# Performance work log

Measured on AMD Instinct MI355X. Metric: run time of the kernel, lower is better.

## Reference

```python
import jax, jax.numpy as jnp
import numpy as np

K = 3  # reassembly kernel size (hardcoded in module)
S = 2  # upsample scale (hardcoded)
PAD = K // 2


def _nearest_up2(t):
    # F.interpolate(scale_factor=2, mode='nearest') on NCHW
    return jnp.repeat(jnp.repeat(t, 2, axis=2), 2, axis=3)


def _patches3x3(t):
    # F.unfold(kernel=3, pad=1) -> [B, C, 9, H, W], k = ki*3 + kj (row-major)
    B, C, H, W = t.shape
    tp = jnp.pad(t, ((0, 0), (0, 0), (PAD, PAD), (PAD, PAD)))
    return jnp.stack([tp[:, :, i:i + H, j:j + W] for i in range(K) for j in range(K)], axis=2)


def setup_inputs() -> dict:
    key = jax.random.key(0)
    k1, k2 = jax.random.split(key)
    x = jax.random.normal(k1, (2, 256, 128, 128), dtype=jnp.float32)
    W_off = jax.random.normal(k2, (2, 1, 5, 5), dtype=jnp.float32) * 1e-3  # normal_init std=0.001
    b_off = jnp.zeros((2,), dtype=jnp.float32)
    return {"x": x, "W_off": W_off, "b_off": b_off}


def reference(x, W_off, b_off):
    B, C, H, W = x.shape
    H2, W2 = S * H, S * W

    mean = jnp.mean(x, axis=1, keepdims=True)  # [B,1,H,W]

    # offset = tanh(conv5x5(nearest_up2(mean))) / 4 -> [B,2,2H,2W]
    mean_up = _nearest_up2(mean)
    off = jax.lax.conv_general_dilated(mean_up, W_off, (1, 1), ((2, 2), (2, 2)))
    offset = jnp.tanh(off + b_off[None, :, None, None]) / 4.0

    # center buffer: pixel_shuffle of [1,8,1,1]; per 2x2 cell, channel 0 varies with j, channel 1 with i
    cell = jnp.array([[[-0.25, 0.25], [-0.25, 0.25]],
                      [[-0.25, -0.25], [0.25, 0.25]]], dtype=x.dtype)  # [2(ch),2(i),2(j)]
    center = jnp.broadcast_to(cell[:, None, :, None, :], (2, H, 2, W, 2)).reshape(2, H2, W2)

    shift = center[None] + offset  # [B,2,2H,2W]

    # neighbor grid: n0 (fast, width) = [-1,0,1]*3 ; n1 (slow, height) = repeat([-1,0,1],3)
    n0 = jnp.tile(jnp.array([-1.0, 0.0, 1.0], dtype=x.dtype), 3)        # [9]
    n1 = jnp.repeat(jnp.array([-1.0, 0.0, 1.0], dtype=x.dtype), 3)      # [9]
    d2 = (shift[:, 0:1] - n0[None, :, None, None]) ** 2 + \
         (shift[:, 1:2] - n1[None, :, None, None]) ** 2                 # [B,9,2H,2W]
    kernels = 1.0 / (d2 + 0.2)

    # grad gating from 3x3 neighborhood of mean
    pm = _patches3x3(mean)[:, 0]            # [B,9,H,W]
    grad = pm - mean                        # broadcast over k
    grad = 1.0 / (grad ** 2 + 1.0)
    logits = _nearest_up2(grad) * kernels   # [B,9,2H,2W]
    kernels = jax.nn.softmax(logits, axis=1)

    # CARAFE: out[b,c,2h+p,2w+q] = sum_k kernels[b,k,2h+p,2w+q] * patches[b,c,k,h,w]
    patches = _patches3x3(x)                        # [B,C,9,H,W]
    Kr = kernels.reshape(B, K * K, H, S, W, S)      # [B,9,H,2,W,2]
    out = jnp.einsum('bkhpwq,bckhw->bchpwq', Kr, patches).reshape(B, C, H2, W2)
    return out
```

## Files before the change

kernel.cpp:

```cpp
#include <hip/hip_runtime.h>
#include <math.h>

#define B 2
#define C 256
#define H 128
#define W 128
#define H2 256
#define W2 256
#define CPT 16
#define TW 16

__global__ __launch_bounds__(1024) void mean_kernel(const float* __restrict__ x,
                                                    float* __restrict__ mean) {
    int bh = blockIdx.x;
    int b = bh / H, h = bh % H;
    int tid = threadIdx.x;
    int g  = tid >> 5;
    int w4 = tid & 31;

    const float4* xb = (const float4*)x + (size_t)b * C * (H * W / 4)
                       + (size_t)h * (W / 4) + w4;
    const size_t cstride = H * W / 4;

    float4 acc = make_float4(0.f, 0.f, 0.f, 0.f);
    #pragma unroll
    for (int i = 0; i < C / 32; ++i) {
        float4 v = xb[(size_t)(g * (C / 32) + i) * cstride];
        acc.x += v.x; acc.y += v.y; acc.z += v.z; acc.w += v.w;
    }

    __shared__ float4 sm[1024];
    sm[tid] = acc;
    __syncthreads();
    for (int s = 16; s >= 1; s >>= 1) {
        if (g < s) {
            float4 o = sm[tid + s * 32];
            acc.x += o.x; acc.y += o.y; acc.z += o.z; acc.w += o.w;
            sm[tid] = acc;
        }
        __syncthreads();
    }
    if (g == 0) {
        const float inv = 1.0f / C;
        float4 m = make_float4(acc.x * inv, acc.y * inv, acc.z * inv, acc.w * inv);
        ((float4*)mean)[(size_t)bh * (W / 4) + w4] = m;
    }
}

__global__ __launch_bounds__(256) void weights_kernel(const float* __restrict__ mean,
                                                      const float* __restrict__ Woff,
                                                      const float* __restrict__ boff,
                                                      float* __restrict__ Kw) {
    __shared__ float sm[10][12];
    __shared__ float sW[50];
    __shared__ float sb[2];

    int b  = blockIdx.z;
    int x0 = blockIdx.x * TW;
    int y0 = blockIdx.y * TW;
    int h0 = y0 >> 1, w0 = x0 >> 1;
    int tid = threadIdx.x;

    if (tid < 100) {
        int lh = tid / 10, lw = tid % 10;
        int hh = h0 - 1 + lh, ww = w0 - 1 + lw;
        sm[lh][lw] = (hh >= 0 && hh < H && ww >= 0 && ww < W)
                         ? mean[(size_t)b * H * W + hh * W + ww] : 0.f;
    }
    if (tid >= 128 && tid < 178) sW[tid - 128] = Woff[tid - 128];
    if (tid >= 192 && tid < 194) sb[tid - 192] = boff[tid - 192];
    __syncthreads();

    int tx = tid & 15, ty = tid >> 4;
    int y = y0 + ty, x = x0 + tx;

    float off0 = 0.f, off1 = 0.f;
    #pragma unroll
    for (int u = 0; u < 5; ++u) {
        int lh = ((y + u - 2) >> 1) - (h0 - 1);
        #pragma unroll
        for (int v = 0; v < 5; ++v) {
            int lw = ((x + v - 2) >> 1) - (w0 - 1);
            float m = sm[lh][lw];
            off0 += m * sW[u * 5 + v];
            off1 += m * sW[25 + u * 5 + v];
        }
    }
    float s0 = tanhf(off0 + sb[0]) * 0.25f + ((x & 1) ? 0.25f : -0.25f);
    float s1 = tanhf(off1 + sb[1]) * 0.25f + ((y & 1) ? 0.25f : -0.25f);

    int lhc = (ty >> 1) + 1;
    int lwc = (tx >> 1) + 1;
    float mc = sm[lhc][lwc];

    float lg[9];
    float mx = -1e30f;
    #pragma unroll
    for (int k = 0; k < 9; ++k) {
        int di = k / 3 - 1, dj = k % 3 - 1;
        float pm = sm[lhc + di][lwc + dj];
        float g = pm - mc;
        float grad = 1.0f / (g * g + 1.0f);
        float d0 = s0 - (float)dj;
        float d1 = s1 - (float)di;
        float kern = 1.0f / (d0 * d0 + d1 * d1 + 0.2f);
        float l = grad * kern;
        lg[k] = l;
        mx = fmaxf(mx, l);
    }
    float sum = 0.f;
    #pragma unroll
    for (int k = 0; k < 9; ++k) { lg[k] = expf(lg[k] - mx); sum += lg[k]; }
    float inv = 1.0f / sum;

    float* o = Kw + (size_t)b * 9 * (H2 * W2) + (size_t)y * W2 + x;
    #pragma unroll
    for (int k = 0; k < 9; ++k) o[(size_t)k * (H2 * W2)] = lg[k] * inv;
}

__global__ __launch_bounds__(256) void carafe_kernel(const float* __restrict__ x,
                                                     const float* __restrict__ Kw,
                                                     float* __restrict__ out) {
    int idx = blockIdx.x * blockDim.x + threadIdx.x;
    int w2 = idx & 63;
    int h  = (idx >> 6) & (H - 1);
    int cg = (idx >> 13) & (C / CPT - 1);
    int b  = idx >> 17;

    int w  = w2 * 2;
    int y0 = 2 * h, x0 = 2 * w;

    const float* kb = Kw + (size_t)b * 9 * (H2 * W2) + (size_t)y0 * W2 + x0;
    float4 wk[2][9];
    #pragma unroll
    for (int k = 0; k < 9; ++k) {
        wk[0][k] = *(const float4*)(kb + (size_t)k * (H2 * W2));
        wk[1][k] = *(const float4*)(kb + (size_t)k * (H2 * W2) + W2);
    }

    int off[3][4]; bool val[3][4];
    #pragma unroll
    for (int r = 0; r < 3; ++r) {
        int hh = h - 1 + r;
        #pragma unroll
        for (int c = 0; c < 4; ++c) {
            int ww = w - 1 + c;
            val[r][c] = (hh >= 0) & (hh < H) & (ww >= 0) & (ww < W);
            off[r][c] = hh * W + ww;
        }
    }

    const float* xb = x   + (size_t)(b * C + cg * CPT) * (H * W);
    float*       ob = out + (size_t)(b * C + cg * CPT) * (H2 * W2)
                          + (size_t)y0 * W2 + x0;

    #pragma unroll 2
    for (int cc = 0; cc < CPT; ++cc) {
        float p[3][4];
        #pragma unroll
        for (int r = 0; r < 3; ++r)
            #pragma unroll
            for (int c = 0; c < 4; ++c)
                p[r][c] = val[r][c] ? xb[off[r][c]] : 0.f;

        #pragma unroll
        for (int pp = 0; pp < 2; ++pp) {
            float4 acc = make_float4(0.f, 0.f, 0.f, 0.f);
            #pragma unroll
            for (int k = 0; k < 9; ++k) {
                int ki = k / 3, kj = k % 3;
                float a  = p[ki][kj];
                float bb = p[ki][kj + 1];
                acc.x += wk[pp][k].x * a;
                acc.y += wk[pp][k].y * a;
                acc.z += wk[pp][k].z * bb;
                acc.w += wk[pp][k].w * bb;
            }
            *(float4*)(ob + (size_t)pp * W2) = acc;
        }
        xb += H * W;
        ob += H2 * W2;
    }
}

extern "C" void kernel_launch(void* const* d_in, const int* in_sizes, int n_in,
                              void* d_out, int out_size, void* d_ws, size_t ws_size,
                              hipStream_t stream) {
    const float* x    = (const float*)d_in[0];
    const float* Woff = (const float*)d_in[1];
    const float* boff = (const float*)d_in[2];
    float* out = (float*)d_out;

    float* mean = (float*)d_ws;
    float* Kw   = mean + (size_t)B * H * W;

    mean_kernel<<<B * H, 1024, 0, stream>>>(x, mean);

    dim3 wgrid(W2 / TW, H2 / TW, B);
    weights_kernel<<<wgrid, 256, 0, stream>>>(mean, Woff, boff, Kw);

    int mt = B * (C / CPT) * H * (W / 2);
    carafe_kernel<<<mt / 256, 256, 0, stream>>>(x, Kw, out);
}
```

Baseline: 176.1 us.

## Use float2 loads with wavefront shuffles for halo, fold boundary masks, nontemporal stores

The CARAFE kernel now loads each input row as one float2 per thread and gets the left and right halo columns from neighbouring lanes via shuffles. Boundary validity is folded into the reassembly weights once, and rows are clamped, so the per-element predicated loads go away. Outputs are written with nontemporal stores so the large output stream does not pollute the cache. The weights kernel switches to hardware reciprocal, fast exp and an exp-based tanh, which trades some accuracy for fewer instructions.

```diff
diff --git a/kernel.cpp b/kernel.cpp
--- a/kernel.cpp
+++ b/kernel.cpp
@@ -10,6 +10,19 @@
 #define CPT 16
 #define TW 16
 
+typedef float vfloat4 __attribute__((ext_vector_type(4)));
+
+__device__ __forceinline__ float frcp(float x) { return __builtin_amdgcn_rcpf(x); }
+__device__ __forceinline__ float fast_tanh(float x) {
+    float e = __expf(2.0f * x);
+    return 1.0f - 2.0f * frcp(e + 1.0f);
+}
+
+__device__ __forceinline__ void nt_store4(float* p, const float4& v) {
+    vfloat4 t; t.x = v.x; t.y = v.y; t.z = v.z; t.w = v.w;
+    __builtin_nontemporal_store(t, (vfloat4*)p);
+}
+
 __global__ __launch_bounds__(1024) void mean_kernel(const float* __restrict__ x,
                                                     float* __restrict__ mean) {
     int bh = blockIdx.x;
@@ -86,8 +99,8 @@
             off1 += m * sW[25 + u * 5 + v];
         }
     }
-    float s0 = tanhf(off0 + sb[0]) * 0.25f + ((x & 1) ? 0.25f : -0.25f);
-    float s1 = tanhf(off1 + sb[1]) * 0.25f + ((y & 1) ? 0.25f : -0.25f);
+    float s0 = fast_tanh(off0 + sb[0]) * 0.25f + ((x & 1) ? 0.25f : -0.25f);
+    float s1 = fast_tanh(off1 + sb[1]) * 0.25f + ((y & 1) ? 0.25f : -0.25f);
 
     int lhc = (ty >> 1) + 1;
     int lwc = (tx >> 1) + 1;
@@ -100,18 +113,18 @@
         int di = k / 3 - 1, dj = k % 3 - 1;
         float pm = sm[lhc + di][lwc + dj];
         float g = pm - mc;
-        float grad = 1.0f / (g * g + 1.0f);
+        float grad = frcp(g * g + 1.0f);
         float d0 = s0 - (float)dj;
         float d1 = s1 - (float)di;
-        float kern = 1.0f / (d0 * d0 + d1 * d1 + 0.2f);
+        float kern = frcp(d0 * d0 + d1 * d1 + 0.2f);
         float l = grad * kern;
         lg[k] = l;
         mx = fmaxf(mx, l);
     }
     float sum = 0.f;
     #pragma unroll
-    for (int k = 0; k < 9; ++k) { lg[k] = expf(lg[k] - mx); sum += lg[k]; }
-    float inv = 1.0f / sum;
+    for (int k = 0; k < 9; ++k) { lg[k] = __expf(lg[k] - mx); sum += lg[k]; }
+    float inv = frcp(sum);
 
     float* o = Kw + (size_t)b * 9 * (H2 * W2) + (size_t)y * W2 + x;
     #pragma unroll
@@ -127,8 +140,8 @@
     int cg = (idx >> 13) & (C / CPT - 1);
     int b  = idx >> 17;
 
-    int w  = w2 * 2;
-    int y0 = 2 * h, x0 = 2 * w;
+    int x0 = 4 * w2;
+    int y0 = 2 * h;
 
     const float* kb = Kw + (size_t)b * 9 * (H2 * W2) + (size_t)y0 * W2 + x0;
     float4 wk[2][9];
@@ -138,48 +151,66 @@
         wk[1][k] = *(const float4*)(kb + (size_t)k * (H2 * W2) + W2);
     }
 
-    int off[3][4]; bool val[3][4];
-    #pragma unroll
-    for (int r = 0; r < 3; ++r) {
-        int hh = h - 1 + r;
+    float rm0 = (h == 0)     ? 0.f : 1.f;
+    float rm2 = (h == H - 1) ? 0.f : 1.f;
+    float cl  = (w2 == 0)    ? 0.f : 1.f;
+    float cr  = (w2 == 63)   ? 0.f : 1.f;
+    #pragma unroll
+    for (int pp = 0; pp < 2; ++pp)
         #pragma unroll
-        for (int c = 0; c < 4; ++c) {
-            int ww = w - 1 + c;
-            val[r][c] = (hh >= 0) & (hh < H) & (ww >= 0) & (ww < W);
-            off[r][c] = hh * W + ww;
-        }
-    }
-
-    const float* xb = x   + (size_t)(b * C + cg * CPT) * (H * W);
-    float*       ob = out + (size_t)(b * C + cg * CPT) * (H2 * W2)
-                          + (size_t)y0 * W2 + x0;
+        for (int k = 0; k < 9; ++k) {
+            int ki = k / 3, kj = k % 3;
+            float r  = (ki == 0) ? rm0 : ((ki == 2) ? rm2 : 1.f);
+            float ma = (kj == 0) ? r * cl : r;
+            float mb = (kj == 2) ? r * cr : r;
+            wk[pp][k].x *= ma; wk[pp][k].y *= ma;
+            wk[pp][k].z *= mb; wk[pp][k].w *= mb;
+        }
+
+    int r0 = (h == 0) ? 0 : h - 1;
+    int r2 = (h == H - 1) ? H - 1 : h + 1;
+
+    const float* xc = x + (size_t)(b * C + cg * CPT) * (H * W);
+    const float2* row0 = (const float2*)(xc + (size_t)r0 * W) + w2;
+    const float2* row1 = (const float2*)(xc + (size_t)h  * W) + w2;
+    const float2* row2 = (const float2*)(xc + (size_t)r2 * W) + w2;
+
+    float* ob = out + (size_t)(b * C + cg * CPT) * (H2 * W2)
+                    + (size_t)y0 * W2 + x0;
 
     #pragma unroll 2
     for (int cc = 0; cc < CPT; ++cc) {
-        float p[3][4];
+        float2 v0 = row0[0];
+        float2 v1 = row1[0];
+        float2 v2 = row2[0];
+
+        float e[3][4];
+        e[0][1] = v0.x; e[0][2] = v0.y;
+        e[1][1] = v1.x; e[1][2] = v1.y;
+        e[2][1] = v2.x; e[2][2] = v2.y;
+        e[0][0] = __shfl_up(v0.y, 1);   e[0][3] = __shfl_down(v0.x, 1);
+        e[1][0] = __shfl_up(v1.y, 1);   e[1][3] = __shfl_down(v1.x, 1);
+        e[2][0] = __shfl_up(v2.y, 1);   e[2][3] = __shfl_down(v2.x, 1);
+
+        float4 a0 = make_float4(0.f, 0.f, 0.f, 0.f);
+        float4 a1 = make_float4(0.f, 0.f, 0.f, 0.f);
         #pragma unroll
-        for (int r = 0; r < 3; ++r)
-            #pragma unroll
-            for (int c = 0; c < 4; ++c)
-                p[r][c] = val[r][c] ? xb[off[r][c]] : 0.f;
-
-        #pragma unroll
-        for (int pp = 0; pp < 2; ++pp) {
-            float4 acc = make_float4(0.f, 0.f, 0.f, 0.f);
-            #pragma unroll
-            for (int k = 0; k < 9; ++k) {
-                int ki = k / 3, kj = k % 3;
-                float a  = p[ki][kj];
-                float bb = p[ki][kj + 1];
-                acc.x += wk[pp][k].x * a;
-                acc.y += wk[pp][k].y * a;
-                acc.z += wk[pp][k].z * bb;
-                acc.w += wk[pp][k].w * bb;
-            }
-            *(float4*)(ob + (size_t)pp * W2) = acc;
-        }
-        xb += H * W;
-        ob += H2 * W2;
+        for (int k = 0; k < 9; ++k) {
+            int ki = k / 3, kj = k % 3;
+            float pa = e[ki][kj];
+            float pb = e[ki][kj + 1];
+            a0.x += wk[0][k].x * pa; a0.y += wk[0][k].y * pa;
+            a0.z += wk[0][k].z * pb; a0.w += wk[0][k].w * pb;
+            a1.x += wk[1][k].x * pa; a1.y += wk[1][k].y * pa;
+            a1.z += wk[1][k].z * pb; a1.w += wk[1][k].w * pb;
+        }
+        nt_store4(ob, a0);
+        nt_store4(ob + W2, a1);
+
+        row0 = (const float2*)((const float*)row0 + H * W);
+        row1 = (const float2*)((const float*)row1 + H * W);
+        row2 = (const float2*)((const float*)row2 + H * W);
+        ob += (size_t)H2 * W2;
     }
 }
 
```

Measured after the change: 173.7 us. About the same (-1.4%).
